# Kernel tuning notes

Hardware: AMD Instinct MI355X
Metric: run time of the kernel (lower is better)

Reference implementation:

```python
import jax, jax.numpy as jnp
import numpy as np
import math

D_MODEL, N_HEADS, D_FF = 1024, 16, 4096
HEAD_DIM = D_MODEL // N_HEADS
BATCH, SEQ = 2, 2048
POPE_BASE = 10000.0
LN_EPS = 1e-5


def setup_inputs() -> dict:
    key = jax.random.key(0)
    ks = jax.random.split(key, 20)
    s = 0.02
    inp = {
        "x": jax.random.normal(ks[0], (BATCH, SEQ, D_MODEL), dtype=jnp.float32),
        "positions": jnp.arange(SEQ, dtype=jnp.int64) if jax.config.jax_enable_x64 else jnp.arange(SEQ, dtype=jnp.int32),
        "Wq": jax.random.normal(ks[1], (D_MODEL, D_MODEL), jnp.float32) * s,
        "bq": jnp.zeros((D_MODEL,), jnp.float32),
        "Wk": jax.random.normal(ks[2], (D_MODEL, D_MODEL), jnp.float32) * s,
        "bk": jnp.zeros((D_MODEL,), jnp.float32),
        "Wv": jax.random.normal(ks[3], (D_MODEL, D_MODEL), jnp.float32) * s,
        "bv": jnp.zeros((D_MODEL,), jnp.float32),
        "Wo": jax.random.normal(ks[4], (D_MODEL, D_MODEL), jnp.float32) * s,
        "bo": jnp.zeros((D_MODEL,), jnp.float32),
        "phase_bias": jax.random.uniform(ks[5], (N_HEADS, HEAD_DIM), jnp.float32,
                                          minval=-2.0 * math.pi, maxval=0.0),
        "freqs": (1.0 / POPE_BASE ** (jnp.arange(HEAD_DIM, dtype=jnp.float32) / HEAD_DIM)),
        "W1": jax.random.normal(ks[6], (D_MODEL, D_FF), jnp.float32) * s,
        "b1": jnp.zeros((D_FF,), jnp.float32),
        "W2": jax.random.normal(ks[7], (D_FF, D_MODEL), jnp.float32) * s,
        "b2": jnp.zeros((D_MODEL,), jnp.float32),
        "g1": jnp.ones((D_MODEL,), jnp.float32),
        "beta1": jnp.zeros((D_MODEL,), jnp.float32),
        "g2": jnp.ones((D_MODEL,), jnp.float32),
        "beta2": jnp.zeros((D_MODEL,), jnp.float32),
    }
    return inp


def _layernorm(x, g, b):
    mu = jnp.mean(x, axis=-1, keepdims=True)
    var = jnp.mean((x - mu) ** 2, axis=-1, keepdims=True)
    return (x - mu) * jax.lax.rsqrt(var + LN_EPS) * g + b


def reference(x, positions, Wq, bq, Wk, bk, Wv, bv, Wo, bo, phase_bias, freqs,
              W1, b1, W2, b2, g1, beta1, g2, beta2):
    B, S, D = x.shape
    H, hd = N_HEADS, HEAD_DIM

    def split_heads(y):  # (B,S,D) -> (B,H,S,hd)
        return y.reshape(B, S, H, hd).transpose(0, 2, 1, 3)

    q = split_heads(x @ Wq + bq)
    k = split_heads(x @ Wk + bk)
    v = split_heads(x @ Wv + bv)

    # --- PoPE: magnitudes via softplus, phases from positions + learned bias ---
    mu_q = jax.nn.softplus(q)
    mu_k = jax.nn.softplus(k)
    pos_phases = positions[:, None].astype(jnp.float32) * freqs[None, :]        # (S,hd)
    phases = pos_phases[None, None, :, :] + phase_bias[None, :, None, :]        # (1,H,S,hd)
    cosp, sinp = jnp.cos(phases), jnp.sin(phases)
    q_pope = jnp.concatenate([mu_q * cosp, mu_q * sinp], axis=-1)               # (B,H,S,2hd)
    k_pope = jnp.concatenate([mu_k * cosp, mu_k * sinp], axis=-1)

    # --- manual causal attention with softmax1 ---
    scale = 1.0 / math.sqrt(2 * hd)  # q.shape[-1] == 2*head_dim under PoPE
    scores = jnp.einsum("bhsd,bhtd->bhst", q_pope, k_pope) * scale
    causal = jnp.triu(jnp.ones((S, S), dtype=bool), k=1)
    scores = jnp.where(causal[None, None], -jnp.inf, scores)
    m = jnp.max(scores, axis=-1, keepdims=True)
    e = jnp.exp(scores - m)
    attn_w = e / (1.0 + jnp.sum(e, axis=-1, keepdims=True))  # softmax1 (as written in source)
    attn = jnp.einsum("bhst,bhtd->bhsd", attn_w, v)

    attn = attn.transpose(0, 2, 1, 3).reshape(B, S, D) @ Wo + bo
    x = _layernorm(x + attn, g1, beta1)
    ff = jax.nn.relu(x @ W1 + b1) @ W2 + b2
    x = _layernorm(x + ff, g2, beta2)
    return x
```

## Files before the change

kernel.cpp:

```cpp
#include <hip/hip_runtime.h>
#include <hip/hip_bf16.h>
#include <math.h>

#define B_   2
#define S_   2048
#define D_   1024
#define H_   16
#define HD_  64
#define DFF_ 4096
#define M_   (B_*S_)
#define SCALE_ 0.08838834764831845f

typedef __attribute__((ext_vector_type(8))) short bf16x8;
typedef __attribute__((ext_vector_type(4))) float f32x4;

#define MFMA16(a,b,c) __builtin_amdgcn_mfma_f32_16x16x32_bf16((a),(b),(c),0,0,0)

__device__ __forceinline__ unsigned short f2b(float f) {
    union { float f; unsigned u; } v; v.f = f;
    return (unsigned short)((v.u + 0x7FFFu + ((v.u >> 16) & 1u)) >> 16);
}
__device__ __forceinline__ float b2f(unsigned short s) {
    union { unsigned u; float f; } v; v.u = ((unsigned)s) << 16;
    return v.f;
}
__device__ __forceinline__ unsigned pk2bf(float a, float b) {
    union { float f; unsigned u; } ua, ub; ua.f = a; ub.f = b;
    return __builtin_amdgcn_perm(ub.u, ua.u, 0x07060302u);
}
__device__ __forceinline__ float softplus_f(float x) {
    return fmaxf(x, 0.f) + log1pf(__expf(-fabsf(x)));
}
__device__ __forceinline__ void g2l16(const void* g, void* l) {
    __builtin_amdgcn_global_load_lds(
        (const __attribute__((address_space(1))) unsigned int*)g,
        (__attribute__((address_space(3))) unsigned int*)l, 16, 0, 0);
}

__global__ __launch_bounds__(256) void prep_kernel(
    const float* __restrict__ x, unsigned short* __restrict__ xb,
    const float* __restrict__ bq, const float* __restrict__ bk,
    const float* __restrict__ bv, float* __restrict__ bqkv,
    const float* __restrict__ Wq, const float* __restrict__ Wk,
    const float* __restrict__ Wv, const float* __restrict__ Wo,
    unsigned short* __restrict__ WqkvT, unsigned short* __restrict__ WoT,
    const float* __restrict__ W1, unsigned short* __restrict__ W1T,
    const float* __restrict__ W2, unsigned short* __restrict__ W2T)
{
    __shared__ float tile[32][33];
    const int bid = blockIdx.x;
    const int tid = threadIdx.x;

    if (bid < 4096) {
        int i = (bid * 256 + tid) * 4;
        float4 v = *(const float4*)&x[i];
        ushort4 o;
        o.x = f2b(v.x); o.y = f2b(v.y); o.z = f2b(v.z); o.w = f2b(v.w);
        *(ushort4*)&xb[i] = o;
        int j = bid * 256 + tid;
        if (j < 3072)
            bqkv[j] = (j < 1024) ? bq[j] : (j < 2048 ? bk[j - 1024] : bv[j - 2048]);
        return;
    }

    const float* W; unsigned short* WT; int K, N, bx, by;
    if (bid < 8192) {
        const int idx = bid - 4096;
        const int z = idx >> 10;
        W  = (z == 0) ? Wq : (z == 1) ? Wk : (z == 2) ? Wv : Wo;
        WT = (z < 3) ? WqkvT + (size_t)z * 1024 * 1024 : WoT;
        K = 1024; N = 1024;
        bx = idx & 31; by = (idx >> 5) & 31;
    } else if (bid < 12288) {
        const int idx = bid - 8192;
        W = W1; WT = W1T; K = 1024; N = 4096;
        bx = idx & 127; by = idx >> 7;
    } else {
        const int idx = bid - 12288;
        W = W2; WT = W2T; K = 4096; N = 1024;
        bx = idx & 31; by = idx >> 5;
    }
    const int n0 = bx * 32, k0 = by * 32;
    const int tx = tid & 31, ty = tid >> 5;
    #pragma unroll
    for (int i = 0; i < 4; i++)
        tile[ty + 8*i][tx] = W[(size_t)(k0 + ty + 8*i) * N + n0 + tx];
    __syncthreads();
    #pragma unroll
    for (int i = 0; i < 4; i++)
        WT[(size_t)(n0 + ty + 8*i) * K + k0 + tx] = f2b(tile[tx][ty + 8*i]);
}

__global__ __launch_bounds__(256) void gemm_bf16_kernel(
    const unsigned short* __restrict__ A,
    const unsigned short* __restrict__ WT,
    const float* __restrict__ bias,
    float* __restrict__ outF, unsigned short* __restrict__ outB,
    int M, int Kslice, int lda, int N, int relu)
{
    __shared__ unsigned short As[2][128 * 64];
    __shared__ unsigned short Bs[2][128 * 64];

    const int tid = threadIdx.x;
    const int w = tid >> 6, lane = tid & 63;
    const int quad = lane >> 4, l16 = lane & 15;

    const int nn = gridDim.x, nm = gridDim.y;
    const int lin = ((int)blockIdx.z * nm + (int)blockIdx.y) * nn + (int)blockIdx.x;
    const int per = (nn * nm * (int)gridDim.z) >> 3;
    const int id  = (lin & 7) * per + (lin >> 3);
    const int zz  = id / (nn * nm);
    const int rem = id - zz * nn * nm;
    const int mt_ = rem / nn, nt_ = rem - mt_ * nn;

    const size_t m0 = (size_t)mt_ * 128, n0 = (size_t)nt_ * 128;
    const int wm = (w >> 1) * 64, wn = (w & 1) * 64;
    const int koff = zz * Kslice;

    const int srow = lane >> 3;
    const int sc   = ((lane & 7) ^ srow) * 8;
    const unsigned short* ga = A  + (m0 + w * 32 + srow) * (size_t)lda + koff + sc;
    const unsigned short* gb = WT + (n0 + w * 32 + srow) * (size_t)lda + koff + sc;
    const size_t rows8 = (size_t)8 * lda;

    f32x4 acc[4][4] = {};
    const int niter = Kslice >> 6;

    #pragma unroll
    for (int j = 0; j < 4; j++) g2l16(ga + j * rows8, &As[0][(w * 32 + j * 8) * 64]);
    #pragma unroll
    for (int j = 0; j < 4; j++) g2l16(gb + j * rows8, &Bs[0][(w * 32 + j * 8) * 64]);

    for (int i = 0; i < niter; i++) {
        __syncthreads();
        if (i + 1 < niter) {
            const int nb = (i + 1) & 1, k0 = (i + 1) << 6;
            #pragma unroll
            for (int j = 0; j < 4; j++)
                g2l16(ga + j * rows8 + k0, &As[nb][(w * 32 + j * 8) * 64]);
            #pragma unroll
            for (int j = 0; j < 4; j++)
                g2l16(gb + j * rows8 + k0, &Bs[nb][(w * 32 + j * 8) * 64]);
        }
        const int buf = i & 1;

        #pragma unroll
        for (int kk = 0; kk < 2; kk++) {
            bf16x8 af[4], bfr[4];
            #pragma unroll
            for (int t = 0; t < 4; t++) {
                const int slot = ((kk * 4 + quad) ^ (l16 & 7)) * 8;
                af[t]  = *(const bf16x8*)&As[buf][(wm + t * 16 + l16) * 64 + slot];
                bfr[t] = *(const bf16x8*)&Bs[buf][(wn + t * 16 + l16) * 64 + slot];
            }
            #pragma unroll
            for (int mt = 0; mt < 4; mt++)
                #pragma unroll
                for (int nt = 0; nt < 4; nt++)
                    acc[mt][nt] = MFMA16(af[mt], bfr[nt], acc[mt][nt]);
        }
    }

    float bv[4];
    #pragma unroll
    for (int nt = 0; nt < 4; nt++)
        bv[nt] = (zz == 0) ? bias[n0 + wn + nt * 16 + l16] : 0.f;

    float* outFz = outF ? outF + (size_t)zz * M * N : nullptr;

    #pragma unroll
    for (int mt = 0; mt < 4; mt++) {
        #pragma unroll
        for (int nt = 0; nt < 4; nt++) {
            const size_t n = n0 + wn + nt * 16 + l16;
            #pragma unroll
            for (int r = 0; r < 4; r++) {
                const size_t m = m0 + wm + mt * 16 + quad * 4 + r;
                float val = acc[mt][nt][r] + bv[nt];
                if (relu) val = fmaxf(val, 0.f);
                const size_t idx = m * N + n;
                if (outFz) outFz[idx] = val;
                if (outB) outB[idx] = f2b(val);
            }
        }
    }
}

__global__ __launch_bounds__(256) void popevt_kernel(
    const unsigned short* __restrict__ qkv,
    const float* __restrict__ phase_bias, const float* __restrict__ freqs,
    unsigned short* __restrict__ qp, unsigned short* __restrict__ kp,
    unsigned short* __restrict__ vt)
{
    __shared__ unsigned short tile[64][68];
    const int bid = blockIdx.x;
    const int tid = threadIdx.x;

    if (bid < 4096) {
        int idx = bid * 256 + tid;
        int d4 = (idx & 15) * 4;
        int s  = (idx >> 4) & (S_ - 1);
        int h  = (idx >> 15) & (H_ - 1);
        int b  = idx >> 19;

        size_t src = (size_t)(b * S_ + s) * 3072 + h * HD_ + d4;
        ushort4 qv = *(const ushort4*)&qkv[src];
        ushort4 kv = *(const ushort4*)&qkv[src + 1024];
        float4 fr = *(const float4*)&freqs[d4];
        float4 pb = *(const float4*)&phase_bias[h * HD_ + d4];
        const float fs = (float)s;

        ushort4 qc4, qs4, kc4, ks4;
        {
            float muq = softplus_f(b2f(qv.x)) * SCALE_, muk = softplus_f(b2f(kv.x));
            float sn, cs; __sincosf(fs * fr.x + pb.x, &sn, &cs);
            qc4.x = f2b(muq * cs); qs4.x = f2b(muq * sn);
            kc4.x = f2b(muk * cs); ks4.x = f2b(muk * sn);
        }
        {
            float muq = softplus_f(b2f(qv.y)) * SCALE_, muk = softplus_f(b2f(kv.y));
            float sn, cs; __sincosf(fs * fr.y + pb.y, &sn, &cs);
            qc4.y = f2b(muq * cs); qs4.y = f2b(muq * sn);
            kc4.y = f2b(muk * cs); ks4.y = f2b(muk * sn);
        }
        {
            float muq = softplus_f(b2f(qv.z)) * SCALE_, muk = softplus_f(b2f(kv.z));
            float sn, cs; __sincosf(fs * fr.z + pb.z, &sn, &cs);
            qc4.z = f2b(muq * cs); qs4.z = f2b(muq * sn);
            kc4.z = f2b(muk * cs); ks4.z = f2b(muk * sn);
        }
        {
            float muq = softplus_f(b2f(qv.w)) * SCALE_, muk = softplus_f(b2f(kv.w));
            float sn, cs; __sincosf(fs * fr.w + pb.w, &sn, &cs);
            qc4.w = f2b(muq * cs); qs4.w = f2b(muq * sn);
            kc4.w = f2b(muk * cs); ks4.w = f2b(muk * sn);
        }

        size_t o = ((size_t)(b * H_ + h) * S_ + s) * 128 + d4;
        *(ushort4*)&qp[o]      = qc4;
        *(ushort4*)&qp[o + 64] = qs4;
        *(ushort4*)&kp[o]      = kc4;
        *(ushort4*)&kp[o + 64] = ks4;
        return;
    }

    const int idx0 = bid - 4096;
    const int bh = idx0 >> 5, b = bh >> 4, h = bh & 15;
    const int s0 = (idx0 & 31) * 64;
    #pragma unroll
    for (int i = 0; i < 4; i++) {
        int idx = i * 256 + tid;
        int s = idx >> 4, d4 = (idx & 15) * 4;
        *(ushort4*)&tile[s][d4] =
            *(const ushort4*)&qkv[(size_t)(b * S_ + s0 + s) * 3072 + 2048 + h * HD_ + d4];
    }
    __syncthreads();
    #pragma unroll
    for (int i = 0; i < 4; i++) {
        int idx = i * 256 + tid;
        int d = idx >> 4, s4 = (idx & 15) * 4;
        ushort4 o;
        o.x = tile[s4][d]; o.y = tile[s4 + 1][d];
        o.z = tile[s4 + 2][d]; o.w = tile[s4 + 3][d];
        *(ushort4*)&vt[((size_t)bh * 64 + d) * S_ + s0 + s4] = o;
    }
}

__global__ __launch_bounds__(512, 4) void attn_mfma_kernel(
    const unsigned short* __restrict__ qp,
    const unsigned short* __restrict__ kp,
    const unsigned short* __restrict__ vt,
    unsigned short* __restrict__ ao)
{
    __shared__ unsigned short kt_lds[2][64][128];
    __shared__ unsigned short vt_lds[2][64][64];
    __shared__ unsigned short p_lds[8][16][72];

    const int tid = threadIdx.x;
    const int w = tid >> 6, lane = tid & 63;
    const int quad = lane >> 4, l16 = lane & 15;
    const int bh = blockIdx.y, b = bh >> 4, h = bh & 15;

    const int a = (blockIdx.z == 0) ? 15 - (int)blockIdx.x : (int)blockIdx.x;
    const int q0b = a * 128;
    const int q0 = q0b + w * 16;

    const unsigned short* qbase = qp + ((size_t)bh * S_ + q0 + l16) * 128 + quad * 8;
    bf16x8 qa[4];
    #pragma unroll
    for (int kc = 0; kc < 4; kc++) qa[kc] = *(const bf16x8*)(qbase + kc * 32);

    const int krow = lane >> 4, kslot = lane & 15;
    const int vrow = lane >> 3, vslot = lane & 7;
    const int kr0 = w * 8 + krow,     kc0 = kslot ^ (kr0 & 15);
    const int kr1 = w * 8 + 4 + krow, kc1 = kslot ^ (kr1 & 15);
    const int vd  = w * 8 + vrow,     vc  = vslot ^ (vd & 7);
    const unsigned short* kg0 = kp + ((size_t)bh * S_ + kr0) * 128 + kc0 * 8;
    const unsigned short* kg1 = kp + ((size_t)bh * S_ + kr1) * 128 + kc1 * 8;
    const unsigned short* vg0 = vt + ((size_t)bh * 64 + vd) * S_ + vc * 8;

    f32x4 o[4] = {};
    float ms = -1e30f, ls = 0.f;

    const int ntiles = 2 * a + 2;

    g2l16(kg0, &kt_lds[0][w * 8][0]);
    g2l16(kg1, &kt_lds[0][w * 8 + 4][0]);
    g2l16(vg0, &vt_lds[0][w * 8][0]);

    for (int ti = 0; ti < ntiles; ti++) {
        const int t0 = ti * 64;
        __syncthreads();
        if (ti + 1 < ntiles) {
            const int nb = (ti + 1) & 1;
            const size_t ko = (size_t)(ti + 1) * (64 * 128);
            const size_t vo = (size_t)(ti + 1) * 64;
            g2l16(kg0 + ko, &kt_lds[nb][w * 8][0]);
            g2l16(kg1 + ko, &kt_lds[nb][w * 8 + 4][0]);
            g2l16(vg0 + vo, &vt_lds[nb][w * 8][0]);
        }
        const int buf = ti & 1;

        if (t0 <= q0 + 15) {
            f32x4 sf[4];
            #pragma unroll
            for (int kg = 0; kg < 4; kg++) {
                f32x4 s = {0, 0, 0, 0};
                const int row = kg * 16 + l16;
                #pragma unroll
                for (int kc = 0; kc < 4; kc++) {
                    const int slot = (kc * 4 + quad) ^ l16;
                    s = MFMA16(*(const bf16x8*)&kt_lds[buf][row][slot * 8], qa[kc], s);
                }
                sf[kg] = s;
            }

            const int qrow = q0 + l16;
            const bool dmask = (t0 + 63 > q0);
            #pragma unroll
            for (int kg = 0; kg < 4; kg++) {
                const int kbase = t0 + kg * 16 + quad * 4;
                float v0 = sf[kg][0], v1 = sf[kg][1], v2 = sf[kg][2], v3 = sf[kg][3];
                if (dmask) {
                    v0 = (kbase     <= qrow) ? v0 : -1e30f;
                    v1 = (kbase + 1 <= qrow) ? v1 : -1e30f;
                    v2 = (kbase + 2 <= qrow) ? v2 : -1e30f;
                    v3 = (kbase + 3 <= qrow) ? v3 : -1e30f;
                }
                ms = fmaxf(ms, fmaxf(fmaxf(v0, v1), fmaxf(v2, v3)));
                const float e0 = __expf(v0), e1 = __expf(v1);
                const float e2 = __expf(v2), e3 = __expf(v3);
                ls += (e0 + e1) + (e2 + e3);
                uint2 pk;
                pk.x = pk2bf(e0, e1);
                pk.y = pk2bf(e2, e3);
                *(uint2*)&p_lds[w][l16][kg * 16 + quad * 4] = pk;
            }
            asm volatile("s_waitcnt lgkmcnt(0)" ::: "memory");
            bf16x8 pa0 = *(const bf16x8*)&p_lds[w][l16][quad * 8];
            bf16x8 pa1 = *(const bf16x8*)&p_lds[w][l16][quad * 8 + 32];

            #pragma unroll
            for (int dg = 0; dg < 4; dg++) {
                const int row = dg * 16 + l16;
                const int s0_ = quad ^ (l16 & 7);
                const int s1_ = (quad + 4) ^ (l16 & 7);
                o[dg] = MFMA16(pa0, *(const bf16x8*)&vt_lds[buf][row][s0_ * 8], o[dg]);
                o[dg] = MFMA16(pa1, *(const bf16x8*)&vt_lds[buf][row][s1_ * 8], o[dg]);
            }
        }
    }

    float mv = ms, lv = ls;
    mv = fmaxf(mv, __shfl_xor(mv, 16, 64)); lv += __shfl_xor(lv, 16, 64);
    mv = fmaxf(mv, __shfl_xor(mv, 32, 64)); lv += __shfl_xor(lv, 32, 64);
    const float inv = 1.f / (__expf(mv) + lv);

    #pragma unroll
    for (int r = 0; r < 4; r++) {
        const float ir = __shfl(inv, quad * 4 + r, 64);
        const int row = q0 + quad * 4 + r;
        const size_t base = (size_t)(b * S_ + row) * D_ + h * HD_ + l16;
        ao[base]      = f2b(o[0][r] * ir);
        ao[base + 16] = f2b(o[1][r] * ir);
        ao[base + 32] = f2b(o[2][r] * ir);
        ao[base + 48] = f2b(o[3][r] * ir);
    }
}

__global__ __launch_bounds__(256) void ln_kernel(
    const float* __restrict__ ya, const float* __restrict__ yb,
    const float* __restrict__ resF, const unsigned short* __restrict__ resB,
    const float* __restrict__ g, const float* __restrict__ beta,
    float* __restrict__ outF, unsigned short* __restrict__ outB)
{
    const int row = blockIdx.x;
    const int tid = threadIdx.x;
    const int c = tid * 4;
    const size_t base = (size_t)row * D_ + c;

    float4 t4 = *(const float4*)(ya + base);
    if (yb) {
        float4 y4 = *(const float4*)(yb + base);
        t4.x += y4.x; t4.y += y4.y; t4.z += y4.z; t4.w += y4.w;
    }
    if (resF) {
        float4 r4 = *(const float4*)(resF + base);
        t4.x += r4.x; t4.y += r4.y; t4.z += r4.z; t4.w += r4.w;
    } else if (resB) {
        ushort4 r4 = *(const ushort4*)(resB + base);
        t4.x += b2f(r4.x); t4.y += b2f(r4.y); t4.z += b2f(r4.z); t4.w += b2f(r4.w);
    }
    float sum   = (t4.x + t4.y) + (t4.z + t4.w);
    float sumsq = (t4.x * t4.x + t4.y * t4.y) + (t4.z * t4.z + t4.w * t4.w);

    #pragma unroll
    for (int off = 32; off >= 1; off >>= 1) {
        sum   += __shfl_xor(sum,   off, 64);
        sumsq += __shfl_xor(sumsq, off, 64);
    }
    __shared__ float rs_[4], rq_[4];
    int w = tid >> 6, lane = tid & 63;
    if (lane == 0) { rs_[w] = sum; rq_[w] = sumsq; }
    __syncthreads();
    float tot  = rs_[0] + rs_[1] + rs_[2] + rs_[3];
    float totq = rq_[0] + rq_[1] + rq_[2] + rq_[3];
    float mu   = tot  * (1.f / D_);
    float var  = totq * (1.f / D_) - mu * mu;
    float rstd = rsqrtf(var + 1e-5f);

    float4 g4 = *(const float4*)(g + c);
    float4 b4 = *(const float4*)(beta + c);
    float4 o4;
    o4.x = (t4.x - mu) * rstd * g4.x + b4.x;
    o4.y = (t4.y - mu) * rstd * g4.y + b4.y;
    o4.z = (t4.z - mu) * rstd * g4.z + b4.z;
    o4.w = (t4.w - mu) * rstd * g4.w + b4.w;
    if (outF) *(float4*)(outF + base) = o4;
    if (outB) {
        ushort4 ob;
        ob.x = f2b(o4.x); ob.y = f2b(o4.y); ob.z = f2b(o4.z); ob.w = f2b(o4.w);
        *(ushort4*)(outB + base) = ob;
    }
}

extern "C" void kernel_launch(void* const* d_in, const int* in_sizes, int n_in,
                              void* d_out, int out_size, void* d_ws, size_t ws_size,
                              hipStream_t stream)
{
    const float* x   = (const float*)d_in[0];
    const float* Wq  = (const float*)d_in[2];
    const float* bq  = (const float*)d_in[3];
    const float* Wk  = (const float*)d_in[4];
    const float* bk  = (const float*)d_in[5];
    const float* Wv  = (const float*)d_in[6];
    const float* bv  = (const float*)d_in[7];
    const float* Wo  = (const float*)d_in[8];
    const float* bo  = (const float*)d_in[9];
    const float* phase_bias = (const float*)d_in[10];
    const float* freqs = (const float*)d_in[11];
    const float* W1  = (const float*)d_in[12];
    const float* b1  = (const float*)d_in[13];
    const float* W2  = (const float*)d_in[14];
    const float* b2  = (const float*)d_in[15];
    const float* g1  = (const float*)d_in[16];
    const float* be1 = (const float*)d_in[17];
    const float* g2  = (const float*)d_in[18];
    const float* be2 = (const float*)d_in[19];
    float* out = (float*)d_out;

    char* base = (char*)d_ws;
    const size_t MiB = 1024 * 1024;
    unsigned short* WqkvT = (unsigned short*)(base);
    unsigned short* WoT   = (unsigned short*)(base + 6  * MiB);
    unsigned short* W1T   = (unsigned short*)(base + 8  * MiB);
    unsigned short* W2T   = (unsigned short*)(base + 16 * MiB);
    float*          bqkv  = (float*)(base + 24 * MiB);
    unsigned short* xb    = (unsigned short*)(base + 25 * MiB);
    unsigned short* qkvb  = (unsigned short*)(base + 33 * MiB);
    unsigned short* qpb   = (unsigned short*)(base + 57 * MiB);
    unsigned short* kpb   = (unsigned short*)(base + 73 * MiB);
    unsigned short* vtb   = (unsigned short*)(base + 89 * MiB);
    float*          po    = (float*)(base + 89 * MiB);
    unsigned short* aob   = xb;
    unsigned short* x1b   = xb;
    unsigned short* hb    = qkvb;
    float*          fo    = po;

    dim3 blk(256);

    prep_kernel<<<dim3(16384), blk, 0, stream>>>(
        x, xb, bq, bk, bv, bqkv, Wq, Wk, Wv, Wo, WqkvT, WoT, W1, W1T, W2, W2T);

    gemm_bf16_kernel<<<dim3(3072 / 128, M_ / 128, 1), blk, 0, stream>>>(
        xb, WqkvT, bqkv, nullptr, qkvb, M_, D_, D_, 3072, 0);

    popevt_kernel<<<dim3(5120), blk, 0, stream>>>(
        qkvb, phase_bias, freqs, qpb, kpb, vtb);

    attn_mfma_kernel<<<dim3(8, B_ * H_, 2), dim3(512), 0, stream>>>(qpb, kpb, vtb, aob);

    gemm_bf16_kernel<<<dim3(D_ / 128, M_ / 128, 2), blk, 0, stream>>>(
        aob, WoT, bo, po, nullptr, M_, D_ / 2, D_, D_, 0);
    ln_kernel<<<dim3(M_), blk, 0, stream>>>(
        po, po + (size_t)M_ * D_, x, nullptr, g1, be1, nullptr, x1b);

    gemm_bf16_kernel<<<dim3(DFF_ / 128, M_ / 128, 1), blk, 0, stream>>>(
        x1b, W1T, b1, nullptr, hb, M_, D_, D_, DFF_, 1);
    gemm_bf16_kernel<<<dim3(D_ / 128, M_ / 128, 2), blk, 0, stream>>>(
        hb, W2T, b2, fo, nullptr, M_, DFF_ / 2, DFF_, D_, 0);
    ln_kernel<<<dim3(M_), blk, 0, stream>>>(
        fo, fo + (size_t)M_ * D_, nullptr, x1b, g2, be2, out, nullptr);
}
```

Measured before the change: 376.7 us.

## Fuse PoPE transform and V transpose into the QKV GEMM epilogue

Replaces the separate QKV GEMM plus the PoPE/V-transpose kernel with one GEMM whose epilogue applies softplus, sincos phase rotation and scaling, then writes qp/kp directly and stores V transposed. This drops the bf16 qkv intermediate round trip through memory and one kernel launch. In exchange the epilogue writes scattered 2-byte stores for Q/K and strided V stores, and softplus now uses a faster but less precise log instead of log1p.

```diff
diff --git a/kernel.cpp b/kernel.cpp
--- a/kernel.cpp
+++ b/kernel.cpp
@@ -30,6 +30,9 @@
 }
 __device__ __forceinline__ float softplus_f(float x) {
     return fmaxf(x, 0.f) + log1pf(__expf(-fabsf(x)));
+}
+__device__ __forceinline__ float softplus_i(float x) {
+    return fmaxf(x, 0.f) + __logf(1.f + __expf(-fabsf(x)));
 }
 __device__ __forceinline__ void g2l16(const void* g, void* l) {
     __builtin_amdgcn_global_load_lds(
@@ -186,83 +189,121 @@
     }
 }
 
-__global__ __launch_bounds__(256) void popevt_kernel(
-    const unsigned short* __restrict__ qkv,
+__global__ __launch_bounds__(256) void gemm_qkv_pope_kernel(
+    const unsigned short* __restrict__ A,
+    const unsigned short* __restrict__ WT,
+    const float* __restrict__ bias,
     const float* __restrict__ phase_bias, const float* __restrict__ freqs,
     unsigned short* __restrict__ qp, unsigned short* __restrict__ kp,
     unsigned short* __restrict__ vt)
 {
-    __shared__ unsigned short tile[64][68];
-    const int bid = blockIdx.x;
+    __shared__ unsigned short As[2][128 * 64];
+    __shared__ unsigned short Bs[2][128 * 64];
+
     const int tid = threadIdx.x;
-
-    if (bid < 4096) {
-        int idx = bid * 256 + tid;
-        int d4 = (idx & 15) * 4;
-        int s  = (idx >> 4) & (S_ - 1);
-        int h  = (idx >> 15) & (H_ - 1);
-        int b  = idx >> 19;
-
-        size_t src = (size_t)(b * S_ + s) * 3072 + h * HD_ + d4;
-        ushort4 qv = *(const ushort4*)&qkv[src];
-        ushort4 kv = *(const ushort4*)&qkv[src + 1024];
-        float4 fr = *(const float4*)&freqs[d4];
-        float4 pb = *(const float4*)&phase_bias[h * HD_ + d4];
-        const float fs = (float)s;
-
-        ushort4 qc4, qs4, kc4, ks4;
-        {
-            float muq = softplus_f(b2f(qv.x)) * SCALE_, muk = softplus_f(b2f(kv.x));
-            float sn, cs; __sincosf(fs * fr.x + pb.x, &sn, &cs);
-            qc4.x = f2b(muq * cs); qs4.x = f2b(muq * sn);
-            kc4.x = f2b(muk * cs); ks4.x = f2b(muk * sn);
-        }
-        {
-            float muq = softplus_f(b2f(qv.y)) * SCALE_, muk = softplus_f(b2f(kv.y));
-            float sn, cs; __sincosf(fs * fr.y + pb.y, &sn, &cs);
-            qc4.y = f2b(muq * cs); qs4.y = f2b(muq * sn);
-            kc4.y = f2b(muk * cs); ks4.y = f2b(muk * sn);
-        }
-        {
-            float muq = softplus_f(b2f(qv.z)) * SCALE_, muk = softplus_f(b2f(kv.z));
-            float sn, cs; __sincosf(fs * fr.z + pb.z, &sn, &cs);
-            qc4.z = f2b(muq * cs); qs4.z = f2b(muq * sn);
-            kc4.z = f2b(muk * cs); ks4.z = f2b(muk * sn);
-        }
-        {
-            float muq = softplus_f(b2f(qv.w)) * SCALE_, muk = softplus_f(b2f(kv.w));
-            float sn, cs; __sincosf(fs * fr.w + pb.w, &sn, &cs);
-            qc4.w = f2b(muq * cs); qs4.w = f2b(muq * sn);
-            kc4.w = f2b(muk * cs); ks4.w = f2b(muk * sn);
-        }
-
-        size_t o = ((size_t)(b * H_ + h) * S_ + s) * 128 + d4;
-        *(ushort4*)&qp[o]      = qc4;
-        *(ushort4*)&qp[o + 64] = qs4;
-        *(ushort4*)&kp[o]      = kc4;
-        *(ushort4*)&kp[o + 64] = ks4;
-        return;
-    }
-
-    const int idx0 = bid - 4096;
-    const int bh = idx0 >> 5, b = bh >> 4, h = bh & 15;
-    const int s0 = (idx0 & 31) * 64;
-    #pragma unroll
-    for (int i = 0; i < 4; i++) {
-        int idx = i * 256 + tid;
-        int s = idx >> 4, d4 = (idx & 15) * 4;
-        *(ushort4*)&tile[s][d4] =
-            *(const ushort4*)&qkv[(size_t)(b * S_ + s0 + s) * 3072 + 2048 + h * HD_ + d4];
-    }
-    __syncthreads();
-    #pragma unroll
-    for (int i = 0; i < 4; i++) {
-        int idx = i * 256 + tid;
-        int d = idx >> 4, s4 = (idx & 15) * 4;
-        ushort4 o;
-        o.x = tile[s4][d]; o.y = tile[s4 + 1][d];
-        o.z = tile[s4 + 2][d]; o.w = tile[s4 + 3][d];
-        *(ushort4*)&vt[((size_t)bh * 64 + d) * S_ + s0 + s4] = o;
+    const int w = tid >> 6, lane = tid & 63;
+    const int quad = lane >> 4, l16 = lane & 15;
+
+    const int nn = gridDim.x, nm = gridDim.y;
+    const int lin = (int)blockIdx.y * nn + (int)blockIdx.x;
+    const int per = (nn * nm) >> 3;
+    const int id  = (lin & 7) * per + (lin >> 3);
+    const int mt_ = id / nn, nt_ = id - mt_ * nn;
+
+    const size_t m0 = (size_t)mt_ * 128, n0 = (size_t)nt_ * 128;
+    const int wm = (w >> 1) * 64, wn = (w & 1) * 64;
+
+    const int srow = lane >> 3;
+    const int sc   = ((lane & 7) ^ srow) * 8;
+    const unsigned short* ga = A  + (m0 + w * 32 + srow) * (size_t)D_ + sc;
+    const unsigned short* gb = WT + (n0 + w * 32 + srow) * (size_t)D_ + sc;
+    const size_t rows8 = (size_t)8 * D_;
+
+    f32x4 acc[4][4] = {};
+    const int niter = D_ >> 6;
+
+    #pragma unroll
+    for (int j = 0; j < 4; j++) g2l16(ga + j * rows8, &As[0][(w * 32 + j * 8) * 64]);
+    #pragma unroll
+    for (int j = 0; j < 4; j++) g2l16(gb + j * rows8, &Bs[0][(w * 32 + j * 8) * 64]);
+
+    for (int i = 0; i < niter; i++) {
+        __syncthreads();
+        if (i + 1 < niter) {
+            const int nb = (i + 1) & 1, k0 = (i + 1) << 6;
+            #pragma unroll
+            for (int j = 0; j < 4; j++)
+                g2l16(ga + j * rows8 + k0, &As[nb][(w * 32 + j * 8) * 64]);
+            #pragma unroll
+            for (int j = 0; j < 4; j++)
+                g2l16(gb + j * rows8 + k0, &Bs[nb][(w * 32 + j * 8) * 64]);
+        }
+        const int buf = i & 1;
+
+        #pragma unroll
+        for (int kk = 0; kk < 2; kk++) {
+            bf16x8 af[4], bfr[4];
+            #pragma unroll
+            for (int t = 0; t < 4; t++) {
+                const int slot = ((kk * 4 + quad) ^ (l16 & 7)) * 8;
+                af[t]  = *(const bf16x8*)&As[buf][(wm + t * 16 + l16) * 64 + slot];
+                bfr[t] = *(const bf16x8*)&Bs[buf][(wn + t * 16 + l16) * 64 + slot];
+            }
+            #pragma unroll
+            for (int mt = 0; mt < 4; mt++)
+                #pragma unroll
+                for (int nt = 0; nt < 4; nt++)
+                    acc[mt][nt] = MFMA16(af[mt], bfr[nt], acc[mt][nt]);
+        }
+    }
+
+    const int nbase = (int)n0 + wn;
+    const int isQ = (nbase < 1024), isV = (nbase >= 2048);
+
+    if (isV) {
+        #pragma unroll
+        for (int nt = 0; nt < 4; nt++) {
+            const int n  = nbase + nt * 16 + l16;
+            const int hv = (n - 2048) >> 6, dv = n & 63;
+            const float bn = bias[n];
+            #pragma unroll
+            for (int mt = 0; mt < 4; mt++) {
+                const int m = (int)m0 + wm + mt * 16 + quad * 4;
+                const int s = m & (S_ - 1), bb = m >> 11;
+                ushort4 vv;
+                vv.x = f2b(acc[mt][nt][0] + bn);
+                vv.y = f2b(acc[mt][nt][1] + bn);
+                vv.z = f2b(acc[mt][nt][2] + bn);
+                vv.w = f2b(acc[mt][nt][3] + bn);
+                *(ushort4*)&vt[((size_t)(bb * H_ + hv) * HD_ + dv) * S_ + s] = vv;
+            }
+        }
+    } else {
+        unsigned short* dst = isQ ? qp : kp;
+        #pragma unroll
+        for (int nt = 0; nt < 4; nt++) {
+            const int n  = nbase + nt * 16 + l16;
+            const int nq = isQ ? n : n - 1024;
+            const int h  = nq >> 6, d = nq & 63;
+            const float fr = freqs[d];
+            const float pb = phase_bias[h * HD_ + d];
+            const float bn = bias[n];
+            #pragma unroll
+            for (int mt = 0; mt < 4; mt++) {
+                #pragma unroll
+                for (int r = 0; r < 4; r++) {
+                    const int m = (int)m0 + wm + mt * 16 + quad * 4 + r;
+                    const int s = m & (S_ - 1), bb = m >> 11;
+                    float mu = softplus_i(acc[mt][nt][r] + bn);
+                    if (isQ) mu *= SCALE_;
+                    float sn, cs;
+                    __sincosf((float)s * fr + pb, &sn, &cs);
+                    const size_t o = ((size_t)(bb * H_ + h) * S_ + s) * 128 + d;
+                    dst[o]      = f2b(mu * cs);
+                    dst[o + 64] = f2b(mu * sn);
+                }
+            }
+        }
     }
 }
 
@@ -492,11 +533,8 @@
     prep_kernel<<<dim3(16384), blk, 0, stream>>>(
         x, xb, bq, bk, bv, bqkv, Wq, Wk, Wv, Wo, WqkvT, WoT, W1, W1T, W2, W2T);
 
-    gemm_bf16_kernel<<<dim3(3072 / 128, M_ / 128, 1), blk, 0, stream>>>(
-        xb, WqkvT, bqkv, nullptr, qkvb, M_, D_, D_, 3072, 0);
-
-    popevt_kernel<<<dim3(5120), blk, 0, stream>>>(
-        qkvb, phase_bias, freqs, qpb, kpb, vtb);
+    gemm_qkv_pope_kernel<<<dim3(3072 / 128, M_ / 128, 1), blk, 0, stream>>>(
+        xb, WqkvT, bqkv, phase_bias, freqs, qpb, kpb, vtb);
 
     attn_mfma_kernel<<<dim3(8, B_ * H_, 2), dim3(512), 0, stream>>>(qpb, kpb, vtb, aob);
 
```

Measured after the change: 366.0 us. 1.03x faster.
